# Kernel tuning notes

Hardware: AMD Instinct MI355X
Metric: run time of the kernel (lower is better)

## Reference

```python
import jax, jax.numpy as jnp
import numpy as np

N = 4096
NHID = 256
K1, K2, K3 = 3072, 2304, 1728


def _layernorm(x, g, b, eps=1e-5):
    m = jnp.mean(x, axis=-1, keepdims=True)
    v = jnp.mean((x - m) ** 2, axis=-1, keepdims=True)
    return (x - m) / jnp.sqrt(v + eps) * g + b


def _gcn(x, A, W, b):
    # PyG GCNConv: add self loops, symmetric norm D^-1/2 (A+I) D^-1/2,
    # messages flow row(source) -> col(target): out[j] = sum_i Anorm[i,j] (xW)[i] + b
    n = A.shape[0]
    A_sl = A + jnp.eye(n, dtype=A.dtype)
    deg = A_sl.sum(0)  # in-degree over col index incl. self loop
    dinv = jnp.where(deg > 0, deg ** -0.5, 0.0)
    An = A_sl * dinv[:, None] * dinv[None, :]
    return An.T @ (x @ W) + b


def _sagpool(x, A, Wp, bp, k):
    score = jnp.tanh(_gcn(x, A, Wp, bp)[:, 0])  # [n]
    vals, perm = jax.lax.top_k(score, k)
    x_new = x[perm] * vals[:, None]
    A_new = A[perm][:, perm]  # induced subgraph of directed edges
    return x_new, A_new


def _readout(x):
    # cat([global_max_pool, global_mean_pool]) for a single graph -> [1, 2*nhid]
    return jnp.concatenate([x.max(0), x.mean(0)])[None, :]


def setup_inputs() -> dict:
    key = jax.random.key(0)
    ks = jax.random.split(key, 10)
    s = 0.05
    return {
        'feature': jax.random.normal(ks[0], (N, 500), jnp.float32),
        'img_info': jax.random.normal(ks[1], (N, 6), jnp.float32),
        'Wp': jax.random.normal(ks[2], (6, 12), jnp.float32) * s,
        'bp': jnp.zeros((12,), jnp.float32),
        'ln_f_g': jnp.ones((500,), jnp.float32),
        'ln_f_b': jnp.zeros((500,), jnp.float32),
        'ln_p_g': jnp.ones((12,), jnp.float32),
        'ln_p_b': jnp.zeros((12,), jnp.float32),
        'W1': jax.random.normal(ks[3], (512, NHID), jnp.float32) * s,
        'b1': jnp.zeros((NHID,), jnp.float32),
        'Wpool1': jax.random.normal(ks[4], (NHID, 1), jnp.float32) * s,
        'bpool1': jnp.zeros((1,), jnp.float32),
        'W2': jax.random.normal(ks[5], (NHID, NHID), jnp.float32) * s,
        'b2': jnp.zeros((NHID,), jnp.float32),
        'Wpool2': jax.random.normal(ks[6], (NHID, 1), jnp.float32) * s,
        'bpool2': jnp.zeros((1,), jnp.float32),
        'W3': jax.random.normal(ks[7], (NHID, NHID), jnp.float32) * s,
        'b3': jnp.zeros((NHID,), jnp.float32),
        'Wpool3': jax.random.normal(ks[8], (NHID, 1), jnp.float32) * s,
        'bpool3': jnp.zeros((1,), jnp.float32),
    }


def reference(feature, img_info, Wp, bp, ln_f_g, ln_f_b, ln_p_g, ln_p_b,
              W1, b1, Wpool1, bpool1, W2, b2, Wpool2, bpool2,
              W3, b3, Wpool3, bpool3):
    # pos embedding + self-attention over nodes
    pos = img_info @ Wp + bp                                  # [N,12]
    att = jax.nn.softmax(pos @ pos.T / jnp.sqrt(12.0), axis=1)  # [N,N]
    pos = att @ pos

    f = _layernorm(feature, ln_f_g, ln_f_b)
    p = _layernorm(pos, ln_p_g, ln_p_b)
    x0 = jnp.concatenate([f, p], axis=1)                      # [N,512]

    # edge construction: upper-triangular directed edges where sqdist < 0.5*max sqdist
    sq = jnp.sum(x0 * x0, axis=1)
    d2 = sq[:, None] - 2.0 * (x0 @ x0.T) + sq[None, :]        # [N,N]
    t = 0.5 * d2.max()
    n = x0.shape[0]
    iu = jnp.triu(jnp.ones((n, n), bool), 1)
    A = jnp.where((d2 < t) & iu, 1.0, 0.0).astype(x0.dtype)

    x = jax.nn.relu(_gcn(x0, A, W1, b1))
    x, A = _sagpool(x, A, Wpool1, bpool1, K1)
    x1 = _readout(x)

    x = jax.nn.relu(_gcn(x, A, W2, b2))
    x, A = _sagpool(x, A, Wpool2, bpool2, K2)
    x2 = _readout(x)

    x = jax.nn.relu(_gcn(x, A, W3, b3))
    x, A = _sagpool(x, A, Wpool3, bpool3, K3)
    x3 = _readout(x)

    return x1 + x2 + x3  # [1, 512]
```

## Files before the change

### kernel.cpp

```cpp
#include <hip/hip_runtime.h>
#include <math.h>

#define NN 4096
#define RB 128

typedef __attribute__((ext_vector_type(8))) short bf16x8;
typedef __attribute__((ext_vector_type(4))) float f32x4;

__device__ __forceinline__ unsigned encf(float f) {
  unsigned u = __float_as_uint(f);
  return (u & 0x80000000u) ? ~u : (u | 0x80000000u);
}
__device__ __forceinline__ float decf(unsigned u) {
  return __uint_as_float((u & 0x80000000u) ? (u ^ 0x80000000u) : ~u);
}
__device__ __forceinline__ unsigned short f2bf(float f) {
  unsigned u = __float_as_uint(f);
  return (unsigned short)((u + 0x7fffu + ((u >> 16) & 1u)) >> 16);
}

__global__ void k_init(float* out, unsigned* dmax) {
  int t = blockIdx.x * 256 + threadIdx.x;
  if (t < 512) out[t] = 0.f;
  if (t == 0) *dmax = 0u;
}

__global__ void k_pos(const float* img, const float* Wp, const float* bp, float* pos) {
  int t = blockIdx.x * 256 + threadIdx.x;
  if (t >= NN * 12) return;
  int i = t / 12, d = t % 12;
  float s = bp[d];
#pragma unroll
  for (int k = 0; k < 6; ++k) s += img[i * 6 + k] * Wp[k * 12 + d];
  pos[t] = s;
}

__global__ __launch_bounds__(256) void k_attn3(const float* pos, float* out) {
  __shared__ float sp[12][256];
  int t = threadIdx.x, lane = t & 63, w = t >> 6;
  int ib = blockIdx.x * 8 + w * 2;
  float pi[2][12];
#pragma unroll
  for (int r = 0; r < 2; ++r)
#pragma unroll
    for (int d = 0; d < 12; ++d) pi[r][d] = pos[(ib + r) * 12 + d] * 0.28867513459481287f;
  float sl[2] = {0.f, 0.f};
  float acc[2][12] = {};
  const float4* p4 = (const float4*)pos;
  for (int kt = 0; kt < NN; kt += 256) {
    __syncthreads();
    int j = kt + t;
    float4 a = p4[j * 3 + 0], b = p4[j * 3 + 1], c = p4[j * 3 + 2];
    sp[0][t] = a.x; sp[1][t] = a.y; sp[2][t] = a.z; sp[3][t] = a.w;
    sp[4][t] = b.x; sp[5][t] = b.y; sp[6][t] = b.z; sp[7][t] = b.w;
    sp[8][t] = c.x; sp[9][t] = c.y; sp[10][t] = c.z; sp[11][t] = c.w;
    __syncthreads();
#pragma unroll
    for (int q = 0; q < 4; ++q) {
      int jj = q * 64 + lane;
      float pj[12];
#pragma unroll
      for (int d = 0; d < 12; ++d) pj[d] = sp[d][jj];
#pragma unroll
      for (int r = 0; r < 2; ++r) {
        float s = 0.f;
#pragma unroll
        for (int d = 0; d < 12; ++d) s = fmaf(pi[r][d], pj[d], s);
        float e = __expf(s);
        sl[r] += e;
#pragma unroll
        for (int d = 0; d < 12; ++d) acc[r][d] = fmaf(e, pj[d], acc[r][d]);
      }
    }
  }
#pragma unroll
  for (int r = 0; r < 2; ++r) {
    float s = sl[r];
#pragma unroll
    for (int o = 32; o > 0; o >>= 1) s += __shfl_xor(s, o);
    float ad[12];
#pragma unroll
    for (int d = 0; d < 12; ++d) {
      ad[d] = acc[r][d];
#pragma unroll
      for (int o = 32; o > 0; o >>= 1) ad[d] += __shfl_xor(ad[d], o);
    }
    if (lane == 0) {
      float inv = 1.f / s;
#pragma unroll
      for (int d = 0; d < 12; ++d) out[(ib + r) * 12 + d] = ad[d] * inv;
    }
  }
}

__global__ __launch_bounds__(256) void k_lnx(const float* f, const float* g, const float* b,
                                             const float* p, const float* pg, const float* pb,
                                             float* x0, unsigned short* x0h, float* sqv) {
  __shared__ float row[512];
  __shared__ float red[256];
  int i = blockIdx.x, t = threadIdx.x;
  float v1 = f[i * 500 + t];
  float v2 = (t < 244) ? f[i * 500 + 256 + t] : 0.f;
  red[t] = v1 + v2; __syncthreads();
  for (int s = 128; s > 0; s >>= 1) { if (t < s) red[t] += red[t + s]; __syncthreads(); }
  float m = red[0] * (1.f / 500.f); __syncthreads();
  float d1 = v1 - m, d2 = v2 - m;
  red[t] = d1 * d1 + ((t < 244) ? d2 * d2 : 0.f); __syncthreads();
  for (int s = 128; s > 0; s >>= 1) { if (t < s) red[t] += red[t + s]; __syncthreads(); }
  float scale = 1.f / sqrtf(red[0] * (1.f / 500.f) + 1e-5f);
  row[t] = d1 * scale * g[t] + b[t];
  if (t < 244) row[256 + t] = d2 * scale * g[256 + t] + b[256 + t];
  if (t >= 244) {
    int tt = t - 244;
    float pv[12], pm = 0.f;
#pragma unroll
    for (int d = 0; d < 12; ++d) { pv[d] = p[i * 12 + d]; pm += pv[d]; }
    pm *= (1.f / 12.f);
    float pvar = 0.f;
#pragma unroll
    for (int d = 0; d < 12; ++d) { float dd = pv[d] - pm; pvar += dd * dd; }
    pvar *= (1.f / 12.f);
    float ps = 1.f / sqrtf(pvar + 1e-5f);
    row[500 + tt] = (pv[tt] - pm) * ps * pg[tt] + pb[tt];
  }
  __syncthreads();
  float a = row[t], c = row[256 + t];
  red[t] = a * a + c * c; __syncthreads();
  for (int s = 128; s > 0; s >>= 1) { if (t < s) red[t] += red[t + s]; __syncthreads(); }
  if (t == 0) sqv[i] = red[0];
  x0[(size_t)i * 512 + t] = a;
  x0[(size_t)i * 512 + 256 + t] = c;
  x0h[(size_t)i * 512 + t] = f2bf(a);
  x0h[(size_t)i * 512 + 256 + t] = f2bf(c);
}

#define BK 64
template <bool MASK>
__global__ __launch_bounds__(256) void k_d2m(const unsigned short* X, const float* sqv,
                                             unsigned* dmax, float* tileMin,
                                             unsigned char* ATm) {
  __shared__ unsigned short As[2][128 * BK];
  __shared__ unsigned short Bs[2][128 * BK];
  __shared__ float wmax[4], wmin[4];
  const int NT = NN / 128;
  int bid0 = blockIdx.x;
  int bid = (bid0 & 7) * 66 + (bid0 >> 3);
  int ti = 0, rem = bid;
  while (rem >= NT - ti) { rem -= NT - ti; ++ti; }
  int tj = ti + rem;
  int t = threadIdx.x, lane = t & 63, w = t >> 6;
  int wr = w >> 1, wc = w & 1;
  const unsigned short* Abase = X + (size_t)ti * 128 * 512;
  const unsigned short* Bbase = X + (size_t)tj * 128 * 512;
  int lr = lane >> 3, lc = lane & 7;

  float thr = 0.f;
  if (MASK) {
    thr = 0.5f * decf(*dmax);
    uint4 z = make_uint4(0u, 0u, 0u, 0u);
    if (ti != tj) {
#pragma unroll
      for (int q0 = 0; q0 < 4; ++q0) {
        int q = t + q0 * 256; int r = q >> 3, c4 = q & 7;
        *(uint4*)(ATm + (size_t)(ti * 128 + r) * NN + tj * 128 + c4 * 16) = z;
      }
    }
    if (tileMin[blockIdx.x] >= thr) {
#pragma unroll
      for (int q0 = 0; q0 < 4; ++q0) {
        int q = t + q0 * 256; int r = q >> 3, c4 = q & 7;
        *(uint4*)(ATm + (size_t)(tj * 128 + r) * NN + ti * 128 + c4 * 16) = z;
      }
      return;
    }
  }

  auto stage = [&](int buf, int k0) {
#pragma unroll
    for (int i = 0; i < 4; ++i) {
      int q = w * 4 + i;
      int r = q * 8 + lr;
      int cs = lc ^ (r & 7);
      __builtin_amdgcn_global_load_lds(
          (const __attribute__((address_space(1))) unsigned int*)(Abase + (size_t)r * 512 + k0 + cs * 8),
          (__attribute__((address_space(3))) unsigned int*)(&As[buf][q * 512]), 16, 0, 0);
      __builtin_amdgcn_global_load_lds(
          (const __attribute__((address_space(1))) unsigned int*)(Bbase + (size_t)r * 512 + k0 + cs * 8),
          (__attribute__((address_space(3))) unsigned int*)(&Bs[buf][q * 512]), 16, 0, 0);
    }
  };

  stage(0, 0);

  f32x4 acc[4][4] = {};
  int rl = lane & 15, kg = lane >> 4;
  for (int step = 0; step < 8; ++step) {
    int cur = step & 1;
    if (step < 7) {
      stage(cur ^ 1, (step + 1) * BK);
      asm volatile("s_waitcnt vmcnt(8)" ::: "memory");
    } else {
      asm volatile("s_waitcnt vmcnt(0)" ::: "memory");
    }
    __builtin_amdgcn_sched_barrier(0);
    __builtin_amdgcn_s_barrier();
#pragma unroll
    for (int ks = 0; ks < 2; ++ks) {
      bf16x8 af[4], bq[4];
#pragma unroll
      for (int f = 0; f < 4; ++f) {
        int rA = wr * 64 + f * 16 + rl;
        af[f] = *(const bf16x8*)(&As[cur][rA * BK + (((ks * 4 + kg) ^ (rA & 7)) << 3)]);
        int rB = wc * 64 + f * 16 + rl;
        bq[f] = *(const bf16x8*)(&Bs[cur][rB * BK + (((ks * 4 + kg) ^ (rB & 7)) << 3)]);
      }
#pragma unroll
      for (int a = 0; a < 4; ++a)
#pragma unroll
        for (int b = 0; b < 4; ++b)
          acc[a][b] = __builtin_amdgcn_mfma_f32_16x16x32_bf16(af[a], bq[b], acc[a][b], 0, 0, 0);
    }
    __builtin_amdgcn_sched_barrier(0);
    __builtin_amdgcn_s_barrier();
  }
  int rbase = ti * 128 + wr * 64 + ((lane >> 4) << 2);
  int cbase = tj * 128 + wc * 64 + (lane & 15);
  if (!MASK) {
    float lm = -1e30f, lmin = 1e30f;
#pragma unroll
    for (int a = 0; a < 4; ++a) {
      float si[4];
#pragma unroll
      for (int r = 0; r < 4; ++r) si[r] = sqv[rbase + a * 16 + r];
#pragma unroll
      for (int b = 0; b < 4; ++b) {
        int gj = cbase + b * 16;
        float sj = sqv[gj];
#pragma unroll
        for (int r = 0; r < 4; ++r) {
          float d2v = si[r] - 2.f * acc[a][b][r] + sj;
          lm = fmaxf(lm, d2v);
          if (rbase + a * 16 + r < gj) lmin = fminf(lmin, d2v);
        }
      }
    }
#pragma unroll
    for (int o = 32; o > 0; o >>= 1) {
      lm = fmaxf(lm, __shfl_xor(lm, o));
      lmin = fminf(lmin, __shfl_xor(lmin, o));
    }
    if (lane == 0) { wmax[w] = lm; wmin[w] = lmin; }
    __syncthreads();
    if (t == 0) {
      atomicMax(dmax, encf(fmaxf(fmaxf(wmax[0], wmax[1]), fmaxf(wmax[2], wmax[3]))));
      tileMin[blockIdx.x] = fminf(fminf(wmin[0], wmin[1]), fminf(wmin[2], wmin[3]));
    }
  } else {
#pragma unroll
    for (int b = 0; b < 4; ++b) {
      int gj = cbase + b * 16;
      float sj = sqv[gj];
#pragma unroll
      for (int a = 0; a < 4; ++a) {
        int gi0 = rbase + a * 16;
        union { unsigned char c[4]; unsigned u; } m4;
#pragma unroll
        for (int r = 0; r < 4; ++r) {
          float d2v = sqv[gi0 + r] - 2.f * acc[a][b][r] + sj;
          m4.c[r] = (d2v < thr && (gi0 + r) < gj) ? 1 : 0;
        }
        *(unsigned*)(ATm + (size_t)gj * NN + gi0) = m4.u;
      }
    }
  }
}

__global__ __launch_bounds__(256) void k_gemm(const float* A, const float* B, const float* dinv,
                                              float* C, int M, int N, int K) {
  __shared__ float As[32][17];
  __shared__ float Bs[16][64];
  int t = threadIdx.x, tx = t & 15, ty = t >> 4;
  int nbx = N >> 6;
  int total = gridDim.x;
  int bid0 = blockIdx.x;
  int bid = (bid0 & 7) * (total >> 3) + (bid0 >> 3);
  int m0 = (bid / nbx) * 32, n0 = (bid % nbx) * 64;
  int ar = t >> 3, ac = (t * 2) & 15;
  int br = t >> 4, bc = (t & 15) * 4;
  float2 ra = *(const float2*)(A + (size_t)(m0 + ar) * K + ac);
  float4 rb = *(const float4*)(B + (size_t)br * N + n0 + bc);
  float acc[2][4] = {};
  for (int k0 = 0; k0 < K; k0 += 16) {
    As[ar][ac] = ra.x; As[ar][ac + 1] = ra.y;
    *(float4*)(&Bs[br][bc]) = rb;
    __syncthreads();
    if (k0 + 16 < K) {
      ra = *(const float2*)(A + (size_t)(m0 + ar) * K + k0 + 16 + ac);
      rb = *(const float4*)(B + (size_t)(k0 + 16 + br) * N + n0 + bc);
    }
#pragma unroll
    for (int kk = 0; kk < 16; ++kk) {
      float av[2], bv[4];
#pragma unroll
      for (int u = 0; u < 2; ++u) av[u] = As[ty * 2 + u][kk];
#pragma unroll
      for (int u = 0; u < 4; ++u) bv[u] = Bs[kk][tx * 4 + u];
#pragma unroll
      for (int a = 0; a < 2; ++a)
#pragma unroll
        for (int b2 = 0; b2 < 4; ++b2) acc[a][b2] = fmaf(av[a], bv[b2], acc[a][b2]);
    }
    __syncthreads();
  }
#pragma unroll
  for (int a = 0; a < 2; ++a) {
    float dv = dinv[m0 + ty * 2 + a];
#pragma unroll
    for (int b2 = 0; b2 < 4; ++b2)
      C[(size_t)(m0 + ty * 2 + a) * N + n0 + tx * 4 + b2] = acc[a][b2] * dv;
  }
}

__global__ __launch_bounds__(256) void k_deg(const unsigned char* ATm, float* dinv, int n) {
  int w = threadIdx.x >> 6, lane = threadIdx.x & 63;
  int j = blockIdx.x * 4 + w;
  if (j >= n) return;
  const uint4* row = (const uint4*)(ATm + (size_t)j * n);
  int sum = 0;
  for (int p = lane; p < n / 16; p += 64) {
    uint4 v = row[p];
    unsigned a = v.x, b = v.y, c = v.z, d = v.w;
    sum += (a & 0xff) + ((a >> 8) & 0xff) + ((a >> 16) & 0xff) + (a >> 24);
    sum += (b & 0xff) + ((b >> 8) & 0xff) + ((b >> 16) & 0xff) + (b >> 24);
    sum += (c & 0xff) + ((c >> 8) & 0xff) + ((c >> 16) & 0xff) + (c >> 24);
    sum += (d & 0xff) + ((d >> 8) & 0xff) + ((d >> 16) & 0xff) + (d >> 24);
  }
  for (int s = 32; s > 0; s >>= 1) sum += __shfl_down(sum, s);
  if (lane == 0) dinv[j] = 1.f / sqrtf((float)(1 + sum));
}

__global__ __launch_bounds__(256) void k_agg(const float* y, const unsigned char* ATm,
                                             const float* dinv, const float* bias,
                                             const float* Wpool, float* out, float* y2, int n) {
  __shared__ unsigned char mrow[256];
  __shared__ int s_any;
  __shared__ float red[256];
  int j = blockIdx.x, t = threadIdx.x;
  float dj = dinv[j];
  float acc = y[(size_t)j * 256 + t];
  if (dj != 1.0f) {
    for (int i0 = 0; i0 < n; i0 += 256) {
      if (t == 0) s_any = 0;
      __syncthreads();
      unsigned char m = ATm[(size_t)j * n + i0 + t];
      mrow[t] = m;
      if (m) s_any = 1;
      __syncthreads();
      if (s_any) {
        for (int u = 0; u < 256; ++u)
          if (mrow[u]) acc += y[(size_t)(i0 + u) * 256 + t];
      }
      __syncthreads();
    }
  }
  float o = fmaxf(dj * acc + bias[t], 0.f);
  out[(size_t)j * 256 + t] = o;
  red[t] = o * Wpool[t]; __syncthreads();
  for (int s = 128; s > 0; s >>= 1) { if (t < s) red[t] += red[t + s]; __syncthreads(); }
  if (t == 0) y2[j] = dj * red[0];
}

__global__ __launch_bounds__(256) void k_scorek(const float* y2, const unsigned char* ATm,
                                                const float* dinv, const float* bp,
                                                float* score, int n) {
  int w = threadIdx.x >> 6, lane = threadIdx.x & 63;
  int j = blockIdx.x * 4 + w;
  if (j >= n) return;
  float dj = dinv[j];
  float s = 0.f;
  if (dj != 1.0f) {
    const uint4* row = (const uint4*)(ATm + (size_t)j * n);
    for (int p = lane; p < n / 16; p += 64) {
      uint4 v = row[p];
      if (v.x | v.y | v.z | v.w) {
        int base = p * 16;
#pragma unroll
        for (int q = 0; q < 4; ++q) {
          unsigned u = (&v.x)[q];
#pragma unroll
          for (int b2 = 0; b2 < 4; ++b2)
            if ((u >> (8 * b2)) & 0xffu) s += y2[base + q * 4 + b2];
        }
      }
    }
    for (int sh = 32; sh > 0; sh >>= 1) s += __shfl_down(s, sh);
  }
  if (lane == 0) score[j] = tanhf(dj * (y2[j] + s) + bp[0]);
}

__global__ __launch_bounds__(1024) void k_topsel(const float* score, int n, int k,
                                                 int* perm, float* vals) {
  __shared__ unsigned keys[4096];
  __shared__ unsigned hist[256];
  __shared__ unsigned s_state[2];
  __shared__ unsigned woff[16];
  int t = threadIdx.x, lane = t & 63, w = t >> 6;
  for (int i = t; i < 4096; i += 1024) keys[i] = (i < n) ? encf(score[i]) : 0u;
  if (t == 0) { s_state[0] = 0u; s_state[1] = (unsigned)k; }
  __syncthreads();

  for (int pass = 0; pass < 4; ++pass) {
    int shift = 24 - pass * 8;
    if (t < 256) hist[t] = 0u;
    __syncthreads();
    unsigned prefix = s_state[0];
    unsigned need = s_state[1];
    unsigned pmask = pass ? (0xFFFFFFFFu << (shift + 8)) : 0u;
    for (int i = t; i < n; i += 1024) {
      unsigned kk = keys[i];
      if ((kk & pmask) == prefix) atomicAdd(&hist[(kk >> shift) & 255u], 1u);
    }
    __syncthreads();
    if (w == 0) {
      unsigned h[4], suf[4];
#pragma unroll
      for (int r = 0; r < 4; ++r) h[r] = hist[lane * 4 + r];
      suf[3] = h[3]; suf[2] = h[2] + suf[3]; suf[1] = h[1] + suf[2]; suf[0] = h[0] + suf[1];
      unsigned lsum = suf[0];
      unsigned s = lsum;
#pragma unroll
      for (int off = 1; off < 64; off <<= 1) {
        unsigned o = __shfl_down(s, off);
        if (lane + off < 64) s += o;
      }
      unsigned Hl = s - lsum;
      int cand = -1; unsigned cumAt = 0, histAt = 0;
#pragma unroll
      for (int r = 0; r < 4; ++r) {
        unsigned c = Hl + suf[r];
        if (c >= need) { cand = lane * 4 + r; cumAt = c; histAt = h[r]; }
      }
      int gmax = cand;
#pragma unroll
      for (int off = 32; off > 0; off >>= 1) {
        int o = __shfl_xor(gmax, off);
        gmax = o > gmax ? o : gmax;
      }
      if (cand == gmax && cand >= 0) {
        s_state[0] = prefix | ((unsigned)cand << shift);
        s_state[1] = need - (cumAt - histAt);
      }
    }
    __syncthreads();
  }
  unsigned cutoff = s_state[0];
  unsigned tcount = s_state[1];
  unsigned G = (unsigned)k - tcount;

  int i0 = t * 4;
  unsigned loc[4], cnt = 0;
#pragma unroll
  for (int r = 0; r < 4; ++r) {
    unsigned kk = keys[i0 + r];
    unsigned g = (kk > cutoff) ? 1u : 0u;
    unsigned e = (kk == cutoff) ? 1u : 0u;
    loc[r] = cnt;
    cnt += (g << 16) | e;
  }
  unsigned inc = cnt;
#pragma unroll
  for (int off = 1; off < 64; off <<= 1) {
    unsigned o = __shfl_up(inc, off);
    if (lane >= off) inc += o;
  }
  if (lane == 63) woff[w] = inc;
  __syncthreads();
  if (t == 0) {
    unsigned run = 0;
    for (int q = 0; q < 16; ++q) { unsigned v = woff[q]; woff[q] = run; run += v; }
  }
  __syncthreads();
  unsigned base = woff[w] + (inc - cnt);
#pragma unroll
  for (int r = 0; r < 4; ++r) {
    unsigned kk = keys[i0 + r];
    unsigned p = base + loc[r];
    if (kk > cutoff) {
      unsigned pos = p >> 16;
      perm[pos] = i0 + r; vals[pos] = decf(kk);
    } else if (kk == cutoff) {
      unsigned pe = p & 0xffffu;
      if (pe < tcount) { perm[G + pe] = i0 + r; vals[G + pe] = decf(kk); }
    }
  }
}

__global__ __launch_bounds__(256) void k_gxp(const float* xg, const int* perm, const float* vals,
                                             float* xp, float* pmax, float* psum, int k) {
  int b = blockIdx.x, t = threadIdx.x;
  float m = -1e30f, s = 0.f;
  for (int r = b; r < k; r += RB) {
    float v = xg[(size_t)perm[r] * 256 + t] * vals[r];
    xp[(size_t)r * 256 + t] = v;
    m = fmaxf(m, v); s += v;
  }
  pmax[b * 256 + t] = m; psum[b * 256 + t] = s;
}
__global__ void k_rfin(const float* pmax, const float* psum, float* out, int k) {
  int t = threadIdx.x;
  float m = -1e30f, s = 0.f;
  for (int q = 0; q < RB; ++q) { m = fmaxf(m, pmax[q * 256 + t]); s += psum[q * 256 + t]; }
  out[t] += m;
  out[256 + t] += s / (float)k;
}

__global__ __launch_bounds__(256) void k_gatherA(const unsigned char* ATold, const int* perm,
                                                 const float* dinvCur,
                                                 unsigned char* ATnew, float* dinvNext,
                                                 int nold, int kn) {
  __shared__ int sperm[4096];
  __shared__ int redi[256];
  int t = threadIdx.x, c = blockIdx.x;
  for (int r = t; r < kn; r += 256) sperm[r] = perm[r];
  __syncthreads();
  int src = sperm[c];
  unsigned char* orow = ATnew + (size_t)c * kn;
  if (dinvCur[src] == 1.0f) {
    uint4 z = make_uint4(0u, 0u, 0u, 0u);
    for (int r = t; r < kn / 16; r += 256) ((uint4*)orow)[r] = z;
    if (t == 0) dinvNext[c] = 1.0f;
    return;
  }
  const unsigned char* row = ATold + (size_t)src * nold;
  int cnt = 0;
  for (int r = t; r < kn; r += 256) { unsigned char v = row[sperm[r]]; orow[r] = v; cnt += v; }
  redi[t] = cnt; __syncthreads();
  for (int s = 128; s > 0; s >>= 1) { if (t < s) redi[t] += redi[t + s]; __syncthreads(); }
  if (t == 0) dinvNext[c] = 1.f / sqrtf((float)(1 + redi[0]));
}

static void run_layer(hipStream_t stream, const float* x_in, int n, int inC,
                      const float* W, const float* b, const float* Wpool, const float* bpool,
                      int k, const unsigned char* ATcur, unsigned char* ATnext,
                      const float* dinvCur, float* dinvNext,
                      float* ybuf, float* xg, float* xp, float* y2,
                      float* score, int* perm, float* vals, float* pmax, float* psum, float* out) {
  k_gemm<<<(n / 32) * 4, 256, 0, stream>>>(x_in, W, dinvCur, ybuf, n, 256, inC);
  k_agg<<<n, 256, 0, stream>>>(ybuf, ATcur, dinvCur, b, Wpool, xg, y2, n);
  k_scorek<<<n / 4, 256, 0, stream>>>(y2, ATcur, dinvCur, bpool, score, n);
  k_topsel<<<1, 1024, 0, stream>>>(score, n, k, perm, vals);
  k_gxp<<<RB, 256, 0, stream>>>(xg, perm, vals, xp, pmax, psum, k);
  k_rfin<<<1, 256, 0, stream>>>(pmax, psum, out, k);
  if (ATnext) k_gatherA<<<k, 256, 0, stream>>>(ATcur, perm, dinvCur, ATnext, dinvNext, n, k);
}

extern "C" void kernel_launch(void* const* d_in, const int* in_sizes, int n_in,
                              void* d_out, int out_size, void* d_ws, size_t ws_size,
                              hipStream_t stream) {
  const float* feature = (const float*)d_in[0];
  const float* img     = (const float*)d_in[1];
  const float* Wp      = (const float*)d_in[2];
  const float* bp      = (const float*)d_in[3];
  const float* ln_f_g  = (const float*)d_in[4];
  const float* ln_f_b  = (const float*)d_in[5];
  const float* ln_p_g  = (const float*)d_in[6];
  const float* ln_p_b  = (const float*)d_in[7];
  const float* W1 = (const float*)d_in[8];   const float* b1 = (const float*)d_in[9];
  const float* Wpool1 = (const float*)d_in[10]; const float* bpool1 = (const float*)d_in[11];
  const float* W2 = (const float*)d_in[12];  const float* b2 = (const float*)d_in[13];
  const float* Wpool2 = (const float*)d_in[14]; const float* bpool2 = (const float*)d_in[15];
  const float* W3 = (const float*)d_in[16];  const float* b3 = (const float*)d_in[17];
  const float* Wpool3 = (const float*)d_in[18]; const float* bpool3 = (const float*)d_in[19];
  float* out = (float*)d_out;
  (void)in_sizes; (void)n_in; (void)out_size; (void)ws_size;

  char* w = (char*)d_ws;
  size_t off = 0;
  auto alloc = [&](size_t bytes) -> char* {
    off = (off + 255) & ~(size_t)255;
    char* p = w + off;
    off += bytes;
    return p;
  };
  float* pos0 = (float*)alloc((size_t)NN * 12 * 4);
  float* pos1 = (float*)alloc((size_t)NN * 12 * 4);
  float* x0   = (float*)alloc((size_t)NN * 512 * 4);
  unsigned short* x0h = (unsigned short*)alloc((size_t)NN * 512 * 2);
  float* sqv  = (float*)alloc((size_t)NN * 4);
  unsigned* dmax = (unsigned*)alloc(4);
  float* tileMin = (float*)alloc(528 * 4);
  float* dinvA = (float*)alloc((size_t)NN * 4);
  float* dinvB = (float*)alloc((size_t)NN * 4);
  float* ybuf = (float*)alloc((size_t)NN * 256 * 4);
  float* xg   = (float*)alloc((size_t)NN * 256 * 4);
  float* xp   = (float*)alloc((size_t)NN * 256 * 4);
  float* y2   = (float*)alloc((size_t)NN * 4);
  float* score= (float*)alloc((size_t)NN * 4);
  int*   perm = (int*)alloc((size_t)NN * 4);
  float* vals = (float*)alloc((size_t)NN * 4);
  float* pmax = (float*)alloc(RB * 256 * 4);
  float* psum = (float*)alloc(RB * 256 * 4);
  unsigned char* ATa = (unsigned char*)alloc((size_t)NN * NN);
  unsigned char* ATb = (unsigned char*)alloc((size_t)3072 * 3072);

  k_init<<<2, 256, 0, stream>>>(out, dmax);
  k_pos<<<(NN * 12 + 255) / 256, 256, 0, stream>>>(img, Wp, bp, pos0);
  k_attn3<<<NN / 8, 256, 0, stream>>>(pos0, pos1);
  k_lnx<<<NN, 256, 0, stream>>>(feature, ln_f_g, ln_f_b, pos1, ln_p_g, ln_p_b, x0, x0h, sqv);

  const int NT = NN / 128, TT = NT * (NT + 1) / 2;
  k_d2m<false><<<TT, 256, 0, stream>>>(x0h, sqv, dmax, tileMin, nullptr);
  k_d2m<true><<<TT, 256, 0, stream>>>(x0h, sqv, dmax, tileMin, ATa);

  k_deg<<<NN / 4, 256, 0, stream>>>(ATa, dinvA, NN);

  run_layer(stream, x0, 4096, 512, W1, b1, Wpool1, bpool1, 3072, ATa, ATb, dinvA, dinvB,
            ybuf, xg, xp, y2, score, perm, vals, pmax, psum, out);
  run_layer(stream, xp, 3072, 256, W2, b2, Wpool2, bpool2, 2304, ATb, ATa, dinvB, dinvA,
            ybuf, xg, xp, y2, score, perm, vals, pmax, psum, out);
  run_layer(stream, xp, 2304, 256, W3, b3, Wpool3, bpool3, 1728, ATa, nullptr, dinvA, nullptr,
            ybuf, xg, xp, y2, score, perm, vals, pmax, psum, out);
}
```

Before: 236.9 us.

## Fuse init, attention+layernorm, degree counting, and readout finalize to cut launches

Folds the init kernel into k_pos and fuses layernorm/concat/sqnorm into the attention kernel's epilogue. Degree counting moves into the masked distance kernel via atomics, which removes the separate k_deg pass over the 16MB adjacency. The readout finalize is merged into k_gxp with a last-block counter, and integer degrees replace stored dinv values. This removes several launches and one full read of the adjacency matrix, at the cost of atomics and one-wave-per-row layernorm work in the attention kernel.

```diff
diff --git a/kernel.cpp b/kernel.cpp
--- a/kernel.cpp
+++ b/kernel.cpp
@@ -19,13 +19,14 @@
   return (unsigned short)((u + 0x7fffu + ((u >> 16) & 1u)) >> 16);
 }
 
-__global__ void k_init(float* out, unsigned* dmax) {
-  int t = blockIdx.x * 256 + threadIdx.x;
-  if (t < 512) out[t] = 0.f;
-  if (t == 0) *dmax = 0u;
-}
-
-__global__ void k_pos(const float* img, const float* Wp, const float* bp, float* pos) {
+__global__ void k_pos(const float* img, const float* Wp, const float* bp, float* pos,
+                      float* out, unsigned* dmax, int* cnt) {
+  if (blockIdx.x == 0) {
+    int tt = threadIdx.x;
+    out[tt] = 0.f; out[256 + tt] = 0.f;
+    if (tt == 0) *dmax = 0u;
+    if (tt < 3) cnt[tt] = 0;
+  }
   int t = blockIdx.x * 256 + threadIdx.x;
   if (t >= NN * 12) return;
   int i = t / 12, d = t % 12;
@@ -35,10 +36,15 @@
   pos[t] = s;
 }
 
-__global__ __launch_bounds__(256) void k_attn3(const float* pos, float* out) {
+__global__ __launch_bounds__(256) void k_attnln(const float* pos, const float* feat,
+                                                const float* g, const float* b,
+                                                const float* pg, const float* pb,
+                                                float* x0, unsigned short* x0h,
+                                                float* sqv, int* degA) {
   __shared__ float sp[12][256];
   int t = threadIdx.x, lane = t & 63, w = t >> 6;
   int ib = blockIdx.x * 8 + w * 2;
+  if (t < 8) degA[blockIdx.x * 8 + t] = 0;
   float pi[2][12];
 #pragma unroll
   for (int r = 0; r < 2; ++r)
@@ -50,9 +56,9 @@
   for (int kt = 0; kt < NN; kt += 256) {
     __syncthreads();
     int j = kt + t;
-    float4 a = p4[j * 3 + 0], b = p4[j * 3 + 1], c = p4[j * 3 + 2];
+    float4 a = p4[j * 3 + 0], bb = p4[j * 3 + 1], c = p4[j * 3 + 2];
     sp[0][t] = a.x; sp[1][t] = a.y; sp[2][t] = a.z; sp[3][t] = a.w;
-    sp[4][t] = b.x; sp[5][t] = b.y; sp[6][t] = b.z; sp[7][t] = b.w;
+    sp[4][t] = bb.x; sp[5][t] = bb.y; sp[6][t] = bb.z; sp[7][t] = bb.w;
     sp[8][t] = c.x; sp[9][t] = c.y; sp[10][t] = c.z; sp[11][t] = c.w;
     __syncthreads();
 #pragma unroll
@@ -75,70 +81,71 @@
   }
 #pragma unroll
   for (int r = 0; r < 2; ++r) {
+    int row = ib + r;
     float s = sl[r];
 #pragma unroll
     for (int o = 32; o > 0; o >>= 1) s += __shfl_xor(s, o);
-    float ad[12];
+    float pa[12];
 #pragma unroll
     for (int d = 0; d < 12; ++d) {
-      ad[d] = acc[r][d];
-#pragma unroll
-      for (int o = 32; o > 0; o >>= 1) ad[d] += __shfl_xor(ad[d], o);
-    }
-    if (lane == 0) {
-      float inv = 1.f / s;
-#pragma unroll
-      for (int d = 0; d < 12; ++d) out[(ib + r) * 12 + d] = ad[d] * inv;
-    }
-  }
-}
-
-__global__ __launch_bounds__(256) void k_lnx(const float* f, const float* g, const float* b,
-                                             const float* p, const float* pg, const float* pb,
-                                             float* x0, unsigned short* x0h, float* sqv) {
-  __shared__ float row[512];
-  __shared__ float red[256];
-  int i = blockIdx.x, t = threadIdx.x;
-  float v1 = f[i * 500 + t];
-  float v2 = (t < 244) ? f[i * 500 + 256 + t] : 0.f;
-  red[t] = v1 + v2; __syncthreads();
-  for (int s = 128; s > 0; s >>= 1) { if (t < s) red[t] += red[t + s]; __syncthreads(); }
-  float m = red[0] * (1.f / 500.f); __syncthreads();
-  float d1 = v1 - m, d2 = v2 - m;
-  red[t] = d1 * d1 + ((t < 244) ? d2 * d2 : 0.f); __syncthreads();
-  for (int s = 128; s > 0; s >>= 1) { if (t < s) red[t] += red[t + s]; __syncthreads(); }
-  float scale = 1.f / sqrtf(red[0] * (1.f / 500.f) + 1e-5f);
-  row[t] = d1 * scale * g[t] + b[t];
-  if (t < 244) row[256 + t] = d2 * scale * g[256 + t] + b[256 + t];
-  if (t >= 244) {
-    int tt = t - 244;
-    float pv[12], pm = 0.f;
-#pragma unroll
-    for (int d = 0; d < 12; ++d) { pv[d] = p[i * 12 + d]; pm += pv[d]; }
+      float ad = acc[r][d];
+#pragma unroll
+      for (int o = 32; o > 0; o >>= 1) ad += __shfl_xor(ad, o);
+      pa[d] = ad;
+    }
+    float inv = 1.f / s;
+#pragma unroll
+    for (int d = 0; d < 12; ++d) pa[d] *= inv;
+    float pm = 0.f;
+#pragma unroll
+    for (int d = 0; d < 12; ++d) pm += pa[d];
     pm *= (1.f / 12.f);
     float pvar = 0.f;
 #pragma unroll
-    for (int d = 0; d < 12; ++d) { float dd = pv[d] - pm; pvar += dd * dd; }
+    for (int d = 0; d < 12; ++d) { float dd = pa[d] - pm; pvar += dd * dd; }
     pvar *= (1.f / 12.f);
     float ps = 1.f / sqrtf(pvar + 1e-5f);
-    row[500 + tt] = (pv[tt] - pm) * ps * pg[tt] + pb[tt];
-  }
-  __syncthreads();
-  float a = row[t], c = row[256 + t];
-  red[t] = a * a + c * c; __syncthreads();
-  for (int s = 128; s > 0; s >>= 1) { if (t < s) red[t] += red[t + s]; __syncthreads(); }
-  if (t == 0) sqv[i] = red[0];
-  x0[(size_t)i * 512 + t] = a;
-  x0[(size_t)i * 512 + 256 + t] = c;
-  x0h[(size_t)i * 512 + t] = f2bf(a);
-  x0h[(size_t)i * 512 + 256 + t] = f2bf(c);
+    float fv[8], lsum = 0.f;
+#pragma unroll
+    for (int q = 0; q < 8; ++q) {
+      int c = lane + q * 64;
+      fv[q] = (c < 500) ? feat[(size_t)row * 500 + c] : 0.f;
+      lsum += fv[q];
+    }
+#pragma unroll
+    for (int o = 32; o > 0; o >>= 1) lsum += __shfl_xor(lsum, o);
+    float m = lsum * (1.f / 500.f);
+    float lvar = 0.f;
+#pragma unroll
+    for (int q = 0; q < 8; ++q) {
+      int c = lane + q * 64;
+      if (c < 500) { float dd = fv[q] - m; lvar += dd * dd; }
+    }
+#pragma unroll
+    for (int o = 32; o > 0; o >>= 1) lvar += __shfl_xor(lvar, o);
+    float scale = 1.f / sqrtf(lvar * (1.f / 500.f) + 1e-5f);
+    float sq = 0.f;
+#pragma unroll
+    for (int q = 0; q < 8; ++q) {
+      int c = lane + q * 64;
+      float val;
+      if (c < 500) val = (fv[q] - m) * scale * g[c] + b[c];
+      else         val = (pa[c - 500] - pm) * ps * pg[c - 500] + pb[c - 500];
+      x0[(size_t)row * 512 + c] = val;
+      x0h[(size_t)row * 512 + c] = f2bf(val);
+      sq += val * val;
+    }
+#pragma unroll
+    for (int o = 32; o > 0; o >>= 1) sq += __shfl_xor(sq, o);
+    if (lane == 0) sqv[row] = sq;
+  }
 }
 
 #define BK 64
 template <bool MASK>
 __global__ __launch_bounds__(256) void k_d2m(const unsigned short* X, const float* sqv,
                                              unsigned* dmax, float* tileMin,
-                                             unsigned char* ATm) {
+                                             unsigned char* ATm, int* deg) {
   __shared__ unsigned short As[2][128 * BK];
   __shared__ unsigned short Bs[2][128 * BK];
   __shared__ float wmax[4], wmin[4];
@@ -260,6 +267,7 @@
     for (int b = 0; b < 4; ++b) {
       int gj = cbase + b * 16;
       float sj = sqv[gj];
+      int rowcnt = 0;
 #pragma unroll
       for (int a = 0; a < 4; ++a) {
         int gi0 = rbase + a * 16;
@@ -267,15 +275,17 @@
 #pragma unroll
         for (int r = 0; r < 4; ++r) {
           float d2v = sqv[gi0 + r] - 2.f * acc[a][b][r] + sj;
-          m4.c[r] = (d2v < thr && (gi0 + r) < gj) ? 1 : 0;
+          unsigned char mv = (d2v < thr && (gi0 + r) < gj) ? 1 : 0;
+          m4.c[r] = mv; rowcnt += mv;
         }
         *(unsigned*)(ATm + (size_t)gj * NN + gi0) = m4.u;
       }
-    }
-  }
-}
-
-__global__ __launch_bounds__(256) void k_gemm(const float* A, const float* B, const float* dinv,
+      if (rowcnt) atomicAdd(&deg[gj], rowcnt);
+    }
+  }
+}
+
+__global__ __launch_bounds__(256) void k_gemm(const float* A, const float* B, const int* deg,
                                               float* C, int M, int N, int K) {
   __shared__ float As[32][17];
   __shared__ float Bs[16][64];
@@ -314,41 +324,24 @@
   }
 #pragma unroll
   for (int a = 0; a < 2; ++a) {
-    float dv = dinv[m0 + ty * 2 + a];
+    float dv = 1.f / sqrtf((float)(1 + deg[m0 + ty * 2 + a]));
 #pragma unroll
     for (int b2 = 0; b2 < 4; ++b2)
       C[(size_t)(m0 + ty * 2 + a) * N + n0 + tx * 4 + b2] = acc[a][b2] * dv;
   }
 }
 
-__global__ __launch_bounds__(256) void k_deg(const unsigned char* ATm, float* dinv, int n) {
-  int w = threadIdx.x >> 6, lane = threadIdx.x & 63;
-  int j = blockIdx.x * 4 + w;
-  if (j >= n) return;
-  const uint4* row = (const uint4*)(ATm + (size_t)j * n);
-  int sum = 0;
-  for (int p = lane; p < n / 16; p += 64) {
-    uint4 v = row[p];
-    unsigned a = v.x, b = v.y, c = v.z, d = v.w;
-    sum += (a & 0xff) + ((a >> 8) & 0xff) + ((a >> 16) & 0xff) + (a >> 24);
-    sum += (b & 0xff) + ((b >> 8) & 0xff) + ((b >> 16) & 0xff) + (b >> 24);
-    sum += (c & 0xff) + ((c >> 8) & 0xff) + ((c >> 16) & 0xff) + (c >> 24);
-    sum += (d & 0xff) + ((d >> 8) & 0xff) + ((d >> 16) & 0xff) + (d >> 24);
-  }
-  for (int s = 32; s > 0; s >>= 1) sum += __shfl_down(sum, s);
-  if (lane == 0) dinv[j] = 1.f / sqrtf((float)(1 + sum));
-}
-
 __global__ __launch_bounds__(256) void k_agg(const float* y, const unsigned char* ATm,
-                                             const float* dinv, const float* bias,
+                                             const int* deg, const float* bias,
                                              const float* Wpool, float* out, float* y2, int n) {
   __shared__ unsigned char mrow[256];
   __shared__ int s_any;
   __shared__ float red[256];
   int j = blockIdx.x, t = threadIdx.x;
-  float dj = dinv[j];
+  int dg = deg[j];
+  float dj = 1.f / sqrtf((float)(1 + dg));
   float acc = y[(size_t)j * 256 + t];
-  if (dj != 1.0f) {
+  if (dg != 0) {
     for (int i0 = 0; i0 < n; i0 += 256) {
       if (t == 0) s_any = 0;
       __syncthreads();
@@ -371,14 +364,15 @@
 }
 
 __global__ __launch_bounds__(256) void k_scorek(const float* y2, const unsigned char* ATm,
-                                                const float* dinv, const float* bp,
+                                                const int* deg, const float* bp,
                                                 float* score, int n) {
   int w = threadIdx.x >> 6, lane = threadIdx.x & 63;
   int j = blockIdx.x * 4 + w;
   if (j >= n) return;
-  float dj = dinv[j];
+  int dg = deg[j];
+  float dj = 1.f / sqrtf((float)(1 + dg));
   float s = 0.f;
-  if (dj != 1.0f) {
+  if (dg != 0) {
     const uint4* row = (const uint4*)(ATm + (size_t)j * n);
     for (int p = lane; p < n / 16; p += 64) {
       uint4 v = row[p];
@@ -496,7 +490,9 @@
 }
 
 __global__ __launch_bounds__(256) void k_gxp(const float* xg, const int* perm, const float* vals,
-                                             float* xp, float* pmax, float* psum, int k) {
+                                             float* xp, float* pmax, float* psum,
+                                             int* cnt, float* out, int k) {
+  __shared__ int isLast;
   int b = blockIdx.x, t = threadIdx.x;
   float m = -1e30f, s = 0.f;
   for (int r = b; r < k; r += RB) {
@@ -505,18 +501,21 @@
     m = fmaxf(m, v); s += v;
   }
   pmax[b * 256 + t] = m; psum[b * 256 + t] = s;
-}
-__global__ void k_rfin(const float* pmax, const float* psum, float* out, int k) {
-  int t = threadIdx.x;
-  float m = -1e30f, s = 0.f;
-  for (int q = 0; q < RB; ++q) { m = fmaxf(m, pmax[q * 256 + t]); s += psum[q * 256 + t]; }
-  out[t] += m;
-  out[256 + t] += s / (float)k;
+  __threadfence();
+  __syncthreads();
+  if (t == 0) isLast = (atomicAdd(cnt, 1) == RB - 1);
+  __syncthreads();
+  if (isLast) {
+    float fm = -1e30f, fs = 0.f;
+    for (int q = 0; q < RB; ++q) { fm = fmaxf(fm, pmax[q * 256 + t]); fs += psum[q * 256 + t]; }
+    out[t] += fm;
+    out[256 + t] += fs / (float)k;
+  }
 }
 
 __global__ __launch_bounds__(256) void k_gatherA(const unsigned char* ATold, const int* perm,
-                                                 const float* dinvCur,
-                                                 unsigned char* ATnew, float* dinvNext,
+                                                 const int* degCur,
+                                                 unsigned char* ATnew, int* degNext,
                                                  int nold, int kn) {
   __shared__ int sperm[4096];
   __shared__ int redi[256];
@@ -525,10 +524,10 @@
   __syncthreads();
   int src = sperm[c];
   unsigned char* orow = ATnew + (size_t)c * kn;
-  if (dinvCur[src] == 1.0f) {
+  if (degCur[src] == 0) {
     uint4 z = make_uint4(0u, 0u, 0u, 0u);
     for (int r = t; r < kn / 16; r += 256) ((uint4*)orow)[r] = z;
-    if (t == 0) dinvNext[c] = 1.0f;
+    if (t == 0) degNext[c] = 0;
     return;
   }
   const unsigned char* row = ATold + (size_t)src * nold;
@@ -536,22 +535,21 @@
   for (int r = t; r < kn; r += 256) { unsigned char v = row[sperm[r]]; orow[r] = v; cnt += v; }
   redi[t] = cnt; __syncthreads();
   for (int s = 128; s > 0; s >>= 1) { if (t < s) redi[t] += redi[t + s]; __syncthreads(); }
-  if (t == 0) dinvNext[c] = 1.f / sqrtf((float)(1 + redi[0]));
+  if (t == 0) degNext[c] = redi[0];
 }
 
 static void run_layer(hipStream_t stream, const float* x_in, int n, int inC,
                       const float* W, const float* b, const float* Wpool, const float* bpool,
                       int k, const unsigned char* ATcur, unsigned char* ATnext,
-                      const float* dinvCur, float* dinvNext,
+                      const int* degCur, int* degNext, int* cnt,
                       float* ybuf, float* xg, float* xp, float* y2,
                       float* score, int* perm, float* vals, float* pmax, float* psum, float* out) {
-  k_gemm<<<(n / 32) * 4, 256, 0, stream>>>(x_in, W, dinvCur, ybuf, n, 256, inC);
-  k_agg<<<n, 256, 0, stream>>>(ybuf, ATcur, dinvCur, b, Wpool, xg, y2, n);
-  k_scorek<<<n / 4, 256, 0, stream>>>(y2, ATcur, dinvCur, bpool, score, n);
+  k_gemm<<<(n / 32) * 4, 256, 0, stream>>>(x_in, W, degCur, ybuf, n, 256, inC);
+  k_agg<<<n, 256, 0, stream>>>(ybuf, ATcur, degCur, b, Wpool, xg, y2, n);
+  k_scorek<<<n / 4, 256, 0, stream>>>(y2, ATcur, degCur, bpool, score, n);
   k_topsel<<<1, 1024, 0, stream>>>(score, n, k, perm, vals);
-  k_gxp<<<RB, 256, 0, stream>>>(xg, perm, vals, xp, pmax, psum, k);
-  k_rfin<<<1, 256, 0, stream>>>(pmax, psum, out, k);
-  if (ATnext) k_gatherA<<<k, 256, 0, stream>>>(ATcur, perm, dinvCur, ATnext, dinvNext, n, k);
+  k_gxp<<<RB, 256, 0, stream>>>(xg, perm, vals, xp, pmax, psum, cnt, out, k);
+  if (ATnext) k_gatherA<<<k, 256, 0, stream>>>(ATcur, perm, degCur, ATnext, degNext, n, k);
 }
 
 extern "C" void kernel_launch(void* const* d_in, const int* in_sizes, int n_in,
@@ -583,14 +581,14 @@
     return p;
   };
   float* pos0 = (float*)alloc((size_t)NN * 12 * 4);
-  float* pos1 = (float*)alloc((size_t)NN * 12 * 4);
   float* x0   = (float*)alloc((size_t)NN * 512 * 4);
   unsigned short* x0h = (unsigned short*)alloc((size_t)NN * 512 * 2);
   float* sqv  = (float*)alloc((size_t)NN * 4);
   unsigned* dmax = (unsigned*)alloc(4);
   float* tileMin = (float*)alloc(528 * 4);
-  float* dinvA = (float*)alloc((size_t)NN * 4);
-  float* dinvB = (float*)alloc((size_t)NN * 4);
+  int* degA = (int*)alloc((size_t)NN * 4);
+  int* degB = (int*)alloc((size_t)NN * 4);
+  int* cnt  = (int*)alloc(3 * 4);
   float* ybuf = (float*)alloc((size_t)NN * 256 * 4);
   float* xg   = (float*)alloc((size_t)NN * 256 * 4);
   float* xp   = (float*)alloc((size_t)NN * 256 * 4);
@@ -603,21 +601,18 @@
   unsigned char* ATa = (unsigned char*)alloc((size_t)NN * NN);
   unsigned char* ATb = (unsigned char*)alloc((size_t)3072 * 3072);
 
-  k_init<<<2, 256, 0, stream>>>(out, dmax);
-  k_pos<<<(NN * 12 + 255) / 256, 256, 0, stream>>>(img, Wp, bp, pos0);
-  k_attn3<<<NN / 8, 256, 0, stream>>>(pos0, pos1);
-  k_lnx<<<NN, 256, 0, stream>>>(feature, ln_f_g, ln_f_b, pos1, ln_p_g, ln_p_b, x0, x0h, sqv);
+  k_pos<<<(NN * 12 + 255) / 256, 256, 0, stream>>>(img, Wp, bp, pos0, out, dmax, cnt);
+  k_attnln<<<NN / 8, 256, 0, stream>>>(pos0, feature, ln_f_g, ln_f_b, ln_p_g, ln_p_b,
+                                       x0, x0h, sqv, degA);
 
   const int NT = NN / 128, TT = NT * (NT + 1) / 2;
-  k_d2m<false><<<TT, 256, 0, stream>>>(x0h, sqv, dmax, tileMin, nullptr);
-  k_d2m<true><<<TT, 256, 0, stream>>>(x0h, sqv, dmax, tileMin, ATa);
-
-  k_deg<<<NN / 4, 256, 0, stream>>>(ATa, dinvA, NN);
-
-  run_layer(stream, x0, 4096, 512, W1, b1, Wpool1, bpool1, 3072, ATa, ATb, dinvA, dinvB,
-            ybuf, xg, xp, y2, score, perm, vals, pmax, psum, out);
-  run_layer(stream, xp, 3072, 256, W2, b2, Wpool2, bpool2, 2304, ATb, ATa, dinvB, dinvA,
-            ybuf, xg, xp, y2, score, perm, vals, pmax, psum, out);
-  run_layer(stream, xp, 2304, 256, W3, b3, Wpool3, bpool3, 1728, ATa, nullptr, dinvA, nullptr,
-            ybuf, xg, xp, y2, score, perm, vals, pmax, psum, out);
-}
+  k_d2m<false><<<TT, 256, 0, stream>>>(x0h, sqv, dmax, tileMin, nullptr, nullptr);
+  k_d2m<true><<<TT, 256, 0, stream>>>(x0h, sqv, dmax, tileMin, ATa, degA);
+
+  run_layer(stream, x0, 4096, 512, W1, b1, Wpool1, bpool1, 3072, ATa, ATb,
+            degA, degB, cnt + 0, ybuf, xg, xp, y2, score, perm, vals, pmax, psum, out);
+  run_layer(stream, xp, 3072, 256, W2, b2, Wpool2, bpool2, 2304, ATb, ATa,
+            degB, degA, cnt + 1, ybuf, xg, xp, y2, score, perm, vals, pmax, psum, out);
+  run_layer(stream, xp, 2304, 256, W3, b3, Wpool3, bpool3, 1728, ATa, nullptr,
+            degA, nullptr, cnt + 2, ybuf, xg, xp, y2, score, perm, vals, pmax, psum, out);
+}
```

After: 257.5 us. 1.09x slower.
